# Optimization experiments

Hardware: AMD Instinct MI355X
Metric: run time of the kernel (lower is better)

The kernel has to match this reference:

```python
import jax, jax.numpy as jnp
import numpy as np

B, T, D, H, O = 16, 1024, 128, 1024, 64
ALPHA = 0.1  # leak rate of the leaky firing-rate cell


def setup_inputs() -> dict:
    key = jax.random.key(0)
    ks = jax.random.split(key, 9)
    s_in, s_rec = 1.0 / np.sqrt(D), 1.0 / np.sqrt(H)
    return {
        "x": jax.random.normal(ks[0], (B, T, D), dtype=jnp.float32),
        "W_in0": jax.random.normal(ks[1], (H, D), dtype=jnp.float32) * s_in,
        "W_rec0": jax.random.normal(ks[2], (H, H), dtype=jnp.float32) * s_rec,
        "b0": jnp.zeros((H,), dtype=jnp.float32),
        "W_in1": jax.random.normal(ks[3], (H, H), dtype=jnp.float32) * s_rec,
        "W_rec1": jax.random.normal(ks[4], (H, H), dtype=jnp.float32) * s_rec,
        "b1": jnp.zeros((H,), dtype=jnp.float32),
        "W_out": jax.random.normal(ks[5], (O, H), dtype=jnp.float32) * s_rec,
        "b_out": jnp.zeros((O,), dtype=jnp.float32),
    }


def reference(x, W_in0, W_rec0, b0, W_in1, W_rec1, b1, W_out, b_out):
    bs = x.shape[0]
    h = W_rec0.shape[0]
    fr0 = jnp.zeros((bs, h), x.dtype)  # init states (torch.zeros layer_states[:,0])
    v0 = jnp.zeros((bs, h), x.dtype)
    fr1 = jnp.zeros((bs, h), x.dtype)
    v1 = jnp.zeros((bs, h), x.dtype)

    def cell(fr, v, u, W_in, W_rec, b):
        # leaky integration: v <- (1-a)v + a(W_in u + W_rec fr + b); fr = tanh(v)
        v_new = (1.0 - ALPHA) * v + ALPHA * (u @ W_in.T + fr @ W_rec.T + b)
        return jnp.tanh(v_new), v_new

    def step(carry, x_t):
        fr0, v0, fr1, v1 = carry
        fr0, v0 = cell(fr0, v0, x_t, W_in0, W_rec0, b0)
        fr1, v1 = cell(fr1, v1, fr0, W_in1, W_rec1, b1)
        return (fr0, v0, fr1, v1), (fr0, fr1)

    xs = jnp.swapaxes(x, 0, 1)  # [T, B, D] for scan over time
    _, (s0, s1) = jax.lax.scan(step, (fr0, v0, fr1, v1), xs)
    states0 = jnp.swapaxes(s0, 0, 1)  # [B, T, H]
    states1 = jnp.swapaxes(s1, 0, 1)  # [B, T, H]
    output = states1 @ W_out.T + b_out  # readout on last layer's state sequence
    return (output, states0, states1)
```

## Files before the change

### kernel.cpp

```cpp
#include <hip/hip_runtime.h>

#define B_ 16
#define T_ 1024
#define D_ 128
#define H_ 1024
#define O_ 64
#define ALPHA_ 0.1f
#define LEAK_ 0.9f
#define GRID_SCAN 256

typedef float f32x4 __attribute__((ext_vector_type(4)));

__global__ __launch_bounds__(256)
void p0_kernel(const float* __restrict__ X, const float* __restrict__ Win0,
               const float* __restrict__ b0, float* __restrict__ P)
{
    __shared__ float Xs[64][68];
    __shared__ float Ws[64][68];
    const int r0 = blockIdx.x * 64;
    const int j0 = blockIdx.y * 64;
    const int tid = threadIdx.x;
    const int ty = tid >> 4, tx = tid & 15;
    float acc[4][4] = {};

    for (int kc = 0; kc < D_; kc += 64) {
        for (int i = tid; i < 64 * 16; i += 256) {
            int row = i >> 4, c = i & 15;
            *(float4*)&Xs[row][c * 4] =
                *(const float4*)&X[(size_t)(r0 + row) * D_ + kc + c * 4];
            *(float4*)&Ws[row][c * 4] =
                *(const float4*)&Win0[(size_t)(j0 + row) * D_ + kc + c * 4];
        }
        __syncthreads();
        #pragma unroll 4
        for (int k = 0; k < 64; k += 4) {
            float4 xr[4], wv[4];
            #pragma unroll
            for (int i = 0; i < 4; ++i) {
                xr[i] = *(const float4*)&Xs[ty * 4 + i][k];
                wv[i] = *(const float4*)&Ws[tx * 4 + i][k];
            }
            #pragma unroll
            for (int i = 0; i < 4; ++i)
                #pragma unroll
                for (int j = 0; j < 4; ++j) {
                    acc[i][j] = fmaf(xr[i].x, wv[j].x, acc[i][j]);
                    acc[i][j] = fmaf(xr[i].y, wv[j].y, acc[i][j]);
                    acc[i][j] = fmaf(xr[i].z, wv[j].z, acc[i][j]);
                    acc[i][j] = fmaf(xr[i].w, wv[j].w, acc[i][j]);
                }
        }
        __syncthreads();
    }
    #pragma unroll
    for (int i = 0; i < 4; ++i) {
        size_t r = (size_t)(r0 + ty * 4 + i);
        #pragma unroll
        for (int j = 0; j < 4; ++j) {
            int jj = j0 + tx * 4 + j;
            P[r * H_ + jj] = ALPHA_ * (acc[i][j] + b0[jj]);
        }
    }
}

#define LDX4(dst, p) \
    asm volatile("global_load_dwordx4 %0, %1, off" : "=v"(dst) : "v"(p))
#define LDSC(dst, p) \
    asm volatile("global_load_dword %0, %1, off sc0 sc1" : "=v"(dst) : "v"(p))
#define VMWAIT(n) asm volatile("s_waitcnt vmcnt(" #n ")" ::: "memory")
#define SB0 __builtin_amdgcn_sched_barrier(0)

#define POLL(ptr, tgtv) do {                                               \
    for (;;) {                                                             \
        unsigned pv_;                                                      \
        LDSC(pv_, (ptr));                                                  \
        VMWAIT(0);                                                         \
        if (__all((int)(pv_ >= (tgtv)))) break;                            \
        __builtin_amdgcn_s_sleep(1);                                       \
    }                                                                      \
    SB0;                                                                   \
} while (0)

#define FMA_A(Ar, r) do {                                                  \
    _Pragma("unroll")                                                      \
    for (int m_ = 0; m_ < 4; ++m_)                                         \
        _Pragma("unroll")                                                  \
        for (int c_ = 0; c_ < 4; ++c_) {                                   \
            const int kk_ = m_ * 4 + c_;                                   \
            const float xa_ = Ar[m_][c_];                                  \
            _Pragma("unroll")                                              \
            for (int j_ = 0; j_ < 4; ++j_) {                               \
                acc0[(r)*4+j_] = fmaf(xa_, wr0[j_][kk_], acc0[(r)*4+j_]);  \
                acc1[(r)*4+j_] = fmaf(xa_, wi1[j_][kk_], acc1[(r)*4+j_]);  \
            }                                                              \
        }                                                                  \
} while (0)

#define FMA_B(Br, r) do {                                                  \
    _Pragma("unroll")                                                      \
    for (int m_ = 0; m_ < 4; ++m_)                                         \
        _Pragma("unroll")                                                  \
        for (int c_ = 0; c_ < 4; ++c_) {                                   \
            const int kk_ = m_ * 4 + c_;                                   \
            const float xb_ = Br[m_][c_];                                  \
            _Pragma("unroll")                                              \
            for (int j_ = 0; j_ < 4; ++j_)                                 \
                acc1[(r)*4+j_] = fmaf(xb_, wr1[j_][kk_], acc1[(r)*4+j_]);  \
        }                                                                  \
} while (0)

__global__ __launch_bounds__(256, 1)
void scan_kernel(const float* __restrict__ Wr0,
                 const float* __restrict__ Wi1,
                 const float* __restrict__ Wr1,
                 const float* __restrict__ b1,
                 float* __restrict__ states0,
                 float* __restrict__ states1,
                 unsigned int* __restrict__ flags)
{
    const int tid  = threadIdx.x;
    const int xcd  = blockIdx.x & 7;
    const int slot = blockIdx.x >> 3;
    const int bg   = xcd >> 1;
    const int jg   = slot * 2 + (xcd & 1);
    const int lane = tid & 63;
    const int w    = tid >> 6;
    const int jq   = lane & 3;
    const int kl   = lane >> 2;
    const int ks   = w * 16 + kl;
    const int k0   = ks << 4;
    const int jbase = jg * 16 + jq * 4;
    const size_t BT = (size_t)T_ * H_;

    float wr0[4][16], wi1[4][16], wr1[4][16];
    #pragma unroll
    for (int j = 0; j < 4; ++j) {
        const float* p0 = Wr0 + (size_t)(jbase + j) * H_ + k0;
        const float* p1 = Wi1 + (size_t)(jbase + j) * H_ + k0;
        const float* p2 = Wr1 + (size_t)(jbase + j) * H_ + k0;
        #pragma unroll
        for (int m = 0; m < 4; ++m) {
            *(float4*)&wr0[j][m * 4] = ((const float4*)p0)[m];
            *(float4*)&wi1[j][m * 4] = ((const float4*)p1)[m];
            *(float4*)&wr1[j][m * 4] = ((const float4*)p2)[m];
        }
    }

    const int o      = tid & 63;
    const int b_loc  = o >> 4, j_loc = o & 15;
    const int gb     = bg * 4 + b_loc;
    const int gj     = jg * 16 + j_loc;
    const int otile  = j_loc >> 2;
    const int oa     = b_loc * 4 + (j_loc & 3);
    float v0 = 0.f, v1 = 0.f;
    const float b1v = b1[gj];

    __shared__ float red[2][4][4][16];

    unsigned* flag0 = flags;
    unsigned* flag1 = flags + 256;
    unsigned* myf0  = flag0 + bg * 64 + jg;
    unsigned* myf1  = flag1 + bg * 64 + jg;
    const unsigned* pf0 = flag0 + bg * 64 + lane;
    const unsigned* pf1 = flag1 + bg * 64 + lane;

    if (tid < 64) {
        size_t oidx = (size_t)gb * BT + gj;
        float pv;
        LDSC(pv, states0 + oidx);
        VMWAIT(0); SB0;
        v0 = pv;
        float fr = tanhf(v0);
        __hip_atomic_store(&states0[oidx], fr, __ATOMIC_RELAXED,
                           __HIP_MEMORY_SCOPE_AGENT);
        VMWAIT(0); SB0;
        if (tid == 0)
            __hip_atomic_store(myf0, 1u, __ATOMIC_RELAXED,
                               __HIP_MEMORY_SCOPE_AGENT);
    }

    for (int it = 1; it <= T_; ++it) {
        const unsigned tgt = (unsigned)it;

        POLL(pf0, tgt);

        float acc0[16], acc1[16];
        #pragma unroll
        for (int a = 0; a < 16; ++a) { acc0[a] = 0.f; acc1[a] = 0.f; }

        const float* sa = states0 + (size_t)(bg * 4) * BT
                        + (size_t)(it - 1) * H_ + k0;
        f32x4 A0[4], A1[4], A2[4], A3[4];
        LDX4(A0[0], sa);          LDX4(A0[1], sa + 4);
        LDX4(A0[2], sa + 8);      LDX4(A0[3], sa + 12);
        LDX4(A1[0], sa + BT);     LDX4(A1[1], sa + BT + 4);
        LDX4(A1[2], sa + BT + 8); LDX4(A1[3], sa + BT + 12);
        LDX4(A2[0], sa + 2*BT);     LDX4(A2[1], sa + 2*BT + 4);
        LDX4(A2[2], sa + 2*BT + 8); LDX4(A2[3], sa + 2*BT + 12);
        LDX4(A3[0], sa + 3*BT);     LDX4(A3[1], sa + 3*BT + 4);
        LDX4(A3[2], sa + 3*BT + 8); LDX4(A3[3], sa + 3*BT + 12);
        float pval = 0.f;
        size_t oidx0 = 0;
        if (tid < 64) {
            const int tp = (it < T_) ? it : (T_ - 1);
            oidx0 = (size_t)gb * BT + (size_t)tp * H_ + gj;
            LDSC(pval, states0 + oidx0);
        }
        VMWAIT(12); SB0;  FMA_A(A0, 0);
        VMWAIT(8);  SB0;  FMA_A(A1, 1);
        VMWAIT(4);  SB0;  FMA_A(A2, 2);
        VMWAIT(0);  SB0;  FMA_A(A3, 3);

        #pragma unroll
        for (int mask = 4; mask < 64; mask <<= 1)
            #pragma unroll
            for (int a = 0; a < 16; ++a)
                acc0[a] += __shfl_xor(acc0[a], mask);
        if (lane < 4)
            #pragma unroll
            for (int a = 0; a < 16; ++a)
                red[0][w][lane][a] = acc0[a];
        __syncthreads();

        if (tid < 64 && it < T_) {
            float s = red[0][0][otile][oa] + red[0][1][otile][oa]
                    + red[0][2][otile][oa] + red[0][3][otile][oa];
            v0 = LEAK_ * v0 + pval + ALPHA_ * s;
            float fr = tanhf(v0);
            __hip_atomic_store(&states0[oidx0], fr, __ATOMIC_RELAXED,
                               __HIP_MEMORY_SCOPE_AGENT);
            VMWAIT(0); SB0;
            if (tid == 0)
                __hip_atomic_store(myf0, (unsigned)(it + 1), __ATOMIC_RELAXED,
                                   __HIP_MEMORY_SCOPE_AGENT);
        }

        if (it >= 2) {
            POLL(pf1, tgt);
            const float* sb = states1 + (size_t)(bg * 4) * BT
                            + (size_t)(it - 2) * H_ + k0;
            f32x4 B0[4], B1r[4], B2r[4], B3r[4];
            LDX4(B0[0], sb);          LDX4(B0[1], sb + 4);
            LDX4(B0[2], sb + 8);      LDX4(B0[3], sb + 12);
            LDX4(B1r[0], sb + BT);     LDX4(B1r[1], sb + BT + 4);
            LDX4(B1r[2], sb + BT + 8); LDX4(B1r[3], sb + BT + 12);
            LDX4(B2r[0], sb + 2*BT);     LDX4(B2r[1], sb + 2*BT + 4);
            LDX4(B2r[2], sb + 2*BT + 8); LDX4(B2r[3], sb + 2*BT + 12);
            LDX4(B3r[0], sb + 3*BT);     LDX4(B3r[1], sb + 3*BT + 4);
            LDX4(B3r[2], sb + 3*BT + 8); LDX4(B3r[3], sb + 3*BT + 12);
            VMWAIT(12); SB0;  FMA_B(B0, 0);
            VMWAIT(8);  SB0;  FMA_B(B1r, 1);
            VMWAIT(4);  SB0;  FMA_B(B2r, 2);
            VMWAIT(0);  SB0;  FMA_B(B3r, 3);
        }

        #pragma unroll
        for (int mask = 4; mask < 64; mask <<= 1)
            #pragma unroll
            for (int a = 0; a < 16; ++a)
                acc1[a] += __shfl_xor(acc1[a], mask);
        if (lane < 4)
            #pragma unroll
            for (int a = 0; a < 16; ++a)
                red[1][w][lane][a] = acc1[a];
        __syncthreads();

        if (tid >= 64 && tid < 128) {
            float s = red[1][0][otile][oa] + red[1][1][otile][oa]
                    + red[1][2][otile][oa] + red[1][3][otile][oa];
            v1 = LEAK_ * v1 + ALPHA_ * (s + b1v);
            float fr = tanhf(v1);
            __hip_atomic_store(&states1[(size_t)gb * BT + (size_t)(it - 1) * H_ + gj],
                               fr, __ATOMIC_RELAXED, __HIP_MEMORY_SCOPE_AGENT);
            VMWAIT(0); SB0;
            if (tid == 64)
                __hip_atomic_store(myf1, (unsigned)(it + 1), __ATOMIC_RELAXED,
                                   __HIP_MEMORY_SCOPE_AGENT);
        }
    }
}

__global__ __launch_bounds__(256)
void out_kernel(const float* __restrict__ S1, const float* __restrict__ Wout,
                const float* __restrict__ bout, float* __restrict__ Out)
{
    __shared__ float Ss[64][36];
    __shared__ float Ws[64][36];
    const int r0 = blockIdx.x * 64;
    const int tid = threadIdx.x;
    const int ty = tid >> 4, tx = tid & 15;
    float acc[4][4] = {};

    for (int kc = 0; kc < H_; kc += 32) {
        for (int i = tid; i < 64 * 8; i += 256) {
            int row = i >> 3, c = i & 7;
            *(float4*)&Ss[row][c * 4] =
                *(const float4*)&S1[(size_t)(r0 + row) * H_ + kc + c * 4];
            *(float4*)&Ws[row][c * 4] =
                *(const float4*)&Wout[(size_t)row * H_ + kc + c * 4];
        }
        __syncthreads();
        #pragma unroll 2
        for (int k = 0; k < 32; k += 4) {
            float4 xr[4], wv[4];
            #pragma unroll
            for (int i = 0; i < 4; ++i) {
                xr[i] = *(const float4*)&Ss[ty * 4 + i][k];
                wv[i] = *(const float4*)&Ws[tx * 4 + i][k];
            }
            #pragma unroll
            for (int i = 0; i < 4; ++i)
                #pragma unroll
                for (int j = 0; j < 4; ++j) {
                    acc[i][j] = fmaf(xr[i].x, wv[j].x, acc[i][j]);
                    acc[i][j] = fmaf(xr[i].y, wv[j].y, acc[i][j]);
                    acc[i][j] = fmaf(xr[i].z, wv[j].z, acc[i][j]);
                    acc[i][j] = fmaf(xr[i].w, wv[j].w, acc[i][j]);
                }
        }
        __syncthreads();
    }
    #pragma unroll
    for (int i = 0; i < 4; ++i) {
        size_t r = (size_t)(r0 + ty * 4 + i);
        #pragma unroll
        for (int j = 0; j < 4; ++j) {
            int oo = tx * 4 + j;
            Out[r * O_ + oo] = acc[i][j] + bout[oo];
        }
    }
}

extern "C" void kernel_launch(void* const* d_in, const int* in_sizes, int n_in,
                              void* d_out, int out_size, void* d_ws, size_t ws_size,
                              hipStream_t stream)
{
    (void)in_sizes; (void)n_in; (void)out_size; (void)ws_size;

    const float* x    = (const float*)d_in[0];
    const float* Win0 = (const float*)d_in[1];
    const float* Wr0  = (const float*)d_in[2];
    const float* b0   = (const float*)d_in[3];
    const float* Wi1  = (const float*)d_in[4];
    const float* Wr1  = (const float*)d_in[5];
    const float* b1   = (const float*)d_in[6];
    const float* Wout = (const float*)d_in[7];
    const float* bout = (const float*)d_in[8];

    float* out     = (float*)d_out;
    float* states0 = out + (size_t)B_ * T_ * O_;
    float* states1 = states0 + (size_t)B_ * T_ * H_;

    unsigned* flags = (unsigned*)d_ws;

    hipMemsetAsync(d_ws, 0, 512 * sizeof(unsigned), stream);

    p0_kernel<<<dim3(B_ * T_ / 64, H_ / 64), 256, 0, stream>>>(x, Win0, b0, states0);

    scan_kernel<<<dim3(GRID_SCAN), dim3(256), 0, stream>>>(
        Wr0, Wi1, Wr1, b1, states0, states1, flags);

    out_kernel<<<dim3(B_ * T_ / 64), 256, 0, stream>>>(states1, Wout, bout, out);
}
```

Baseline: 4.977 ms.

## Split recurrent scan into separate layer-0 and layer-1 block groups

Doubles the scan grid and gives each layer its own set of persistent blocks. Layer-0 blocks only do the W_rec0 matvec and publish states0. Layer-1 blocks poll both flag sets and then do the W_in1 and W_rec1 products, so layer 1 trails layer 0 in a pipeline instead of sitting on its serial path. The costs are twice as many co-resident blocks (launch bounds raised to 2 per CU) and extra cross-block flag polling; if all blocks cannot be resident at once, the spin-waits could deadlock.

```diff
diff --git a/kernel.cpp b/kernel.cpp
--- a/kernel.cpp
+++ b/kernel.cpp
@@ -7,7 +7,7 @@
 #define O_ 64
 #define ALPHA_ 0.1f
 #define LEAK_ 0.9f
-#define GRID_SCAN 256
+#define GRID_SCAN 512
 
 typedef float f32x4 __attribute__((ext_vector_type(4)));
 
@@ -70,46 +70,54 @@
 #define VMWAIT(n) asm volatile("s_waitcnt vmcnt(" #n ")" ::: "memory")
 #define SB0 __builtin_amdgcn_sched_barrier(0)
 
-#define POLL(ptr, tgtv) do {                                               \
+#define POLL1F(pa_, tgtv) do {                                             \
     for (;;) {                                                             \
-        unsigned pv_;                                                      \
-        LDSC(pv_, (ptr));                                                  \
+        unsigned va_;                                                      \
+        LDSC(va_, (pa_));                                                  \
         VMWAIT(0);                                                         \
-        if (__all((int)(pv_ >= (tgtv)))) break;                            \
+        if (__all((int)(va_ >= (tgtv)))) break;                            \
         __builtin_amdgcn_s_sleep(1);                                       \
     }                                                                      \
     SB0;                                                                   \
 } while (0)
 
-#define FMA_A(Ar, r) do {                                                  \
+#define POLL2F(pa_, pb_, tgtv) do {                                        \
+    for (;;) {                                                             \
+        unsigned va_, vb_;                                                 \
+        LDSC(va_, (pa_));                                                  \
+        LDSC(vb_, (pb_));                                                  \
+        VMWAIT(0);                                                         \
+        if (__all((int)((va_ >= (tgtv)) & (vb_ >= (tgtv))))) break;        \
+        __builtin_amdgcn_s_sleep(1);                                       \
+    }                                                                      \
+    SB0;                                                                   \
+} while (0)
+
+#define FMA_G(Ar, r, W) do {                                               \
     _Pragma("unroll")                                                      \
     for (int m_ = 0; m_ < 4; ++m_)                                         \
         _Pragma("unroll")                                                  \
         for (int c_ = 0; c_ < 4; ++c_) {                                   \
             const int kk_ = m_ * 4 + c_;                                   \
-            const float xa_ = Ar[m_][c_];                                  \
+            const float x_ = Ar[m_][c_];                                   \
             _Pragma("unroll")                                              \
-            for (int j_ = 0; j_ < 4; ++j_) {                               \
-                acc0[(r)*4+j_] = fmaf(xa_, wr0[j_][kk_], acc0[(r)*4+j_]);  \
-                acc1[(r)*4+j_] = fmaf(xa_, wi1[j_][kk_], acc1[(r)*4+j_]);  \
-            }                                                              \
+            for (int j_ = 0; j_ < 4; ++j_)                                 \
+                acc[(r)*4+j_] = fmaf(x_, W[j_][kk_], acc[(r)*4+j_]);       \
         }                                                                  \
 } while (0)
 
-#define FMA_B(Br, r) do {                                                  \
-    _Pragma("unroll")                                                      \
-    for (int m_ = 0; m_ < 4; ++m_)                                         \
-        _Pragma("unroll")                                                  \
-        for (int c_ = 0; c_ < 4; ++c_) {                                   \
-            const int kk_ = m_ * 4 + c_;                                   \
-            const float xb_ = Br[m_][c_];                                  \
-            _Pragma("unroll")                                              \
-            for (int j_ = 0; j_ < 4; ++j_)                                 \
-                acc1[(r)*4+j_] = fmaf(xb_, wr1[j_][kk_], acc1[(r)*4+j_]);  \
-        }                                                                  \
+#define LOAD_ROWS(Rv, base) do {                                           \
+    LDX4(Rv##0[0], (base));              LDX4(Rv##0[1], (base) + 4);       \
+    LDX4(Rv##0[2], (base) + 8);          LDX4(Rv##0[3], (base) + 12);      \
+    LDX4(Rv##1[0], (base) + BT);         LDX4(Rv##1[1], (base) + BT + 4);  \
+    LDX4(Rv##1[2], (base) + BT + 8);     LDX4(Rv##1[3], (base) + BT + 12); \
+    LDX4(Rv##2[0], (base) + 2*BT);       LDX4(Rv##2[1], (base) + 2*BT + 4);\
+    LDX4(Rv##2[2], (base) + 2*BT + 8);   LDX4(Rv##2[3], (base) + 2*BT + 12);\
+    LDX4(Rv##3[0], (base) + 3*BT);       LDX4(Rv##3[1], (base) + 3*BT + 4);\
+    LDX4(Rv##3[2], (base) + 3*BT + 8);   LDX4(Rv##3[3], (base) + 3*BT + 12);\
 } while (0)
 
-__global__ __launch_bounds__(256, 1)
+__global__ __launch_bounds__(256, 2)
 void scan_kernel(const float* __restrict__ Wr0,
                  const float* __restrict__ Wi1,
                  const float* __restrict__ Wr1,
@@ -118,9 +126,12 @@
                  float* __restrict__ states1,
                  unsigned int* __restrict__ flags)
 {
-    const int tid  = threadIdx.x;
-    const int xcd  = blockIdx.x & 7;
-    const int slot = blockIdx.x >> 3;
+    const int tid   = threadIdx.x;
+    const int blk   = blockIdx.x;
+    const int eng   = blk >> 8;
+    const int inner = blk & 255;
+    const int xcd  = inner & 7;
+    const int slot = inner >> 3;
     const int bg   = xcd >> 1;
     const int jg   = slot * 2 + (xcd & 1);
     const int lane = tid & 63;
@@ -132,150 +143,166 @@
     const int jbase = jg * 16 + jq * 4;
     const size_t BT = (size_t)T_ * H_;
 
-    float wr0[4][16], wi1[4][16], wr1[4][16];
-    #pragma unroll
-    for (int j = 0; j < 4; ++j) {
-        const float* p0 = Wr0 + (size_t)(jbase + j) * H_ + k0;
-        const float* p1 = Wi1 + (size_t)(jbase + j) * H_ + k0;
-        const float* p2 = Wr1 + (size_t)(jbase + j) * H_ + k0;
-        #pragma unroll
-        for (int m = 0; m < 4; ++m) {
-            *(float4*)&wr0[j][m * 4] = ((const float4*)p0)[m];
-            *(float4*)&wi1[j][m * 4] = ((const float4*)p1)[m];
-            *(float4*)&wr1[j][m * 4] = ((const float4*)p2)[m];
-        }
-    }
-
     const int o      = tid & 63;
     const int b_loc  = o >> 4, j_loc = o & 15;
     const int gb     = bg * 4 + b_loc;
     const int gj     = jg * 16 + j_loc;
     const int otile  = j_loc >> 2;
     const int oa     = b_loc * 4 + (j_loc & 3);
-    float v0 = 0.f, v1 = 0.f;
-    const float b1v = b1[gj];
-
-    __shared__ float red[2][4][4][16];
+
+    __shared__ float red[4][4][16];
 
     unsigned* flag0 = flags;
     unsigned* flag1 = flags + 256;
-    unsigned* myf0  = flag0 + bg * 64 + jg;
-    unsigned* myf1  = flag1 + bg * 64 + jg;
     const unsigned* pf0 = flag0 + bg * 64 + lane;
     const unsigned* pf1 = flag1 + bg * 64 + lane;
 
-    if (tid < 64) {
-        size_t oidx = (size_t)gb * BT + gj;
-        float pv;
-        LDSC(pv, states0 + oidx);
-        VMWAIT(0); SB0;
-        v0 = pv;
-        float fr = tanhf(v0);
-        __hip_atomic_store(&states0[oidx], fr, __ATOMIC_RELAXED,
-                           __HIP_MEMORY_SCOPE_AGENT);
-        VMWAIT(0); SB0;
-        if (tid == 0)
-            __hip_atomic_store(myf0, 1u, __ATOMIC_RELAXED,
-                               __HIP_MEMORY_SCOPE_AGENT);
-    }
-
-    for (int it = 1; it <= T_; ++it) {
-        const unsigned tgt = (unsigned)it;
-
-        POLL(pf0, tgt);
-
-        float acc0[16], acc1[16];
+    if (eng == 0) {
+        float wr0[4][16];
         #pragma unroll
-        for (int a = 0; a < 16; ++a) { acc0[a] = 0.f; acc1[a] = 0.f; }
-
-        const float* sa = states0 + (size_t)(bg * 4) * BT
-                        + (size_t)(it - 1) * H_ + k0;
-        f32x4 A0[4], A1[4], A2[4], A3[4];
-        LDX4(A0[0], sa);          LDX4(A0[1], sa + 4);
-        LDX4(A0[2], sa + 8);      LDX4(A0[3], sa + 12);
-        LDX4(A1[0], sa + BT);     LDX4(A1[1], sa + BT + 4);
-        LDX4(A1[2], sa + BT + 8); LDX4(A1[3], sa + BT + 12);
-        LDX4(A2[0], sa + 2*BT);     LDX4(A2[1], sa + 2*BT + 4);
-        LDX4(A2[2], sa + 2*BT + 8); LDX4(A2[3], sa + 2*BT + 12);
-        LDX4(A3[0], sa + 3*BT);     LDX4(A3[1], sa + 3*BT + 4);
-        LDX4(A3[2], sa + 3*BT + 8); LDX4(A3[3], sa + 3*BT + 12);
-        float pval = 0.f;
-        size_t oidx0 = 0;
+        for (int j = 0; j < 4; ++j) {
+            const float* p0 = Wr0 + (size_t)(jbase + j) * H_ + k0;
+            #pragma unroll
+            for (int m = 0; m < 4; ++m)
+                *(float4*)&wr0[j][m * 4] = ((const float4*)p0)[m];
+        }
+        unsigned* myf0 = flag0 + bg * 64 + jg;
+        float v0 = 0.f;
+
         if (tid < 64) {
-            const int tp = (it < T_) ? it : (T_ - 1);
-            oidx0 = (size_t)gb * BT + (size_t)tp * H_ + gj;
-            LDSC(pval, states0 + oidx0);
-        }
-        VMWAIT(12); SB0;  FMA_A(A0, 0);
-        VMWAIT(8);  SB0;  FMA_A(A1, 1);
-        VMWAIT(4);  SB0;  FMA_A(A2, 2);
-        VMWAIT(0);  SB0;  FMA_A(A3, 3);
-
-        #pragma unroll
-        for (int mask = 4; mask < 64; mask <<= 1)
-            #pragma unroll
-            for (int a = 0; a < 16; ++a)
-                acc0[a] += __shfl_xor(acc0[a], mask);
-        if (lane < 4)
-            #pragma unroll
-            for (int a = 0; a < 16; ++a)
-                red[0][w][lane][a] = acc0[a];
-        __syncthreads();
-
-        if (tid < 64 && it < T_) {
-            float s = red[0][0][otile][oa] + red[0][1][otile][oa]
-                    + red[0][2][otile][oa] + red[0][3][otile][oa];
-            v0 = LEAK_ * v0 + pval + ALPHA_ * s;
+            size_t oidx = (size_t)gb * BT + gj;
+            float pv;
+            LDSC(pv, states0 + oidx);
+            VMWAIT(0); SB0;
+            v0 = pv;
             float fr = tanhf(v0);
-            __hip_atomic_store(&states0[oidx0], fr, __ATOMIC_RELAXED,
+            __hip_atomic_store(&states0[oidx], fr, __ATOMIC_RELAXED,
                                __HIP_MEMORY_SCOPE_AGENT);
             VMWAIT(0); SB0;
             if (tid == 0)
-                __hip_atomic_store(myf0, (unsigned)(it + 1), __ATOMIC_RELAXED,
+                __hip_atomic_store(myf0, 1u, __ATOMIC_RELAXED,
                                    __HIP_MEMORY_SCOPE_AGENT);
         }
 
-        if (it >= 2) {
-            POLL(pf1, tgt);
-            const float* sb = states1 + (size_t)(bg * 4) * BT
-                            + (size_t)(it - 2) * H_ + k0;
-            f32x4 B0[4], B1r[4], B2r[4], B3r[4];
-            LDX4(B0[0], sb);          LDX4(B0[1], sb + 4);
-            LDX4(B0[2], sb + 8);      LDX4(B0[3], sb + 12);
-            LDX4(B1r[0], sb + BT);     LDX4(B1r[1], sb + BT + 4);
-            LDX4(B1r[2], sb + BT + 8); LDX4(B1r[3], sb + BT + 12);
-            LDX4(B2r[0], sb + 2*BT);     LDX4(B2r[1], sb + 2*BT + 4);
-            LDX4(B2r[2], sb + 2*BT + 8); LDX4(B2r[3], sb + 2*BT + 12);
-            LDX4(B3r[0], sb + 3*BT);     LDX4(B3r[1], sb + 3*BT + 4);
-            LDX4(B3r[2], sb + 3*BT + 8); LDX4(B3r[3], sb + 3*BT + 12);
-            VMWAIT(12); SB0;  FMA_B(B0, 0);
-            VMWAIT(8);  SB0;  FMA_B(B1r, 1);
-            VMWAIT(4);  SB0;  FMA_B(B2r, 2);
-            VMWAIT(0);  SB0;  FMA_B(B3r, 3);
-        }
-
+        for (int it = 1; it < T_; ++it) {
+            POLL1F(pf0, (unsigned)it);
+
+            float acc[16];
+            #pragma unroll
+            for (int a = 0; a < 16; ++a) acc[a] = 0.f;
+
+            const float* sa = states0 + (size_t)(bg * 4) * BT
+                            + (size_t)(it - 1) * H_ + k0;
+            f32x4 A0[4], A1[4], A2[4], A3[4];
+            LOAD_ROWS(A, sa);
+            float pval = 0.f;
+            size_t oidx0 = 0;
+            if (tid < 64) {
+                oidx0 = (size_t)gb * BT + (size_t)it * H_ + gj;
+                LDSC(pval, states0 + oidx0);
+            }
+            VMWAIT(12); SB0;  FMA_G(A0, 0, wr0);
+            VMWAIT(8);  SB0;  FMA_G(A1, 1, wr0);
+            VMWAIT(4);  SB0;  FMA_G(A2, 2, wr0);
+            VMWAIT(0);  SB0;  FMA_G(A3, 3, wr0);
+
+            #pragma unroll
+            for (int mask = 4; mask < 64; mask <<= 1)
+                #pragma unroll
+                for (int a = 0; a < 16; ++a)
+                    acc[a] += __shfl_xor(acc[a], mask);
+            if (lane < 4)
+                #pragma unroll
+                for (int a = 0; a < 16; ++a)
+                    red[w][lane][a] = acc[a];
+            __syncthreads();
+
+            if (tid < 64) {
+                float s = red[0][otile][oa] + red[1][otile][oa]
+                        + red[2][otile][oa] + red[3][otile][oa];
+                v0 = LEAK_ * v0 + pval + ALPHA_ * s;
+                float fr = tanhf(v0);
+                __hip_atomic_store(&states0[oidx0], fr, __ATOMIC_RELAXED,
+                                   __HIP_MEMORY_SCOPE_AGENT);
+                VMWAIT(0); SB0;
+                if (tid == 0)
+                    __hip_atomic_store(myf0, (unsigned)(it + 1),
+                                       __ATOMIC_RELAXED,
+                                       __HIP_MEMORY_SCOPE_AGENT);
+            }
+        }
+    } else {
+        float wi1[4][16], wr1[4][16];
         #pragma unroll
-        for (int mask = 4; mask < 64; mask <<= 1)
-            #pragma unroll
-            for (int a = 0; a < 16; ++a)
-                acc1[a] += __shfl_xor(acc1[a], mask);
-        if (lane < 4)
-            #pragma unroll
-            for (int a = 0; a < 16; ++a)
-                red[1][w][lane][a] = acc1[a];
-        __syncthreads();
-
-        if (tid >= 64 && tid < 128) {
-            float s = red[1][0][otile][oa] + red[1][1][otile][oa]
-                    + red[1][2][otile][oa] + red[1][3][otile][oa];
-            v1 = LEAK_ * v1 + ALPHA_ * (s + b1v);
-            float fr = tanhf(v1);
-            __hip_atomic_store(&states1[(size_t)gb * BT + (size_t)(it - 1) * H_ + gj],
-                               fr, __ATOMIC_RELAXED, __HIP_MEMORY_SCOPE_AGENT);
-            VMWAIT(0); SB0;
-            if (tid == 64)
-                __hip_atomic_store(myf1, (unsigned)(it + 1), __ATOMIC_RELAXED,
+        for (int j = 0; j < 4; ++j) {
+            const float* p1 = Wi1 + (size_t)(jbase + j) * H_ + k0;
+            const float* p2 = Wr1 + (size_t)(jbase + j) * H_ + k0;
+            #pragma unroll
+            for (int m = 0; m < 4; ++m) {
+                *(float4*)&wi1[j][m * 4] = ((const float4*)p1)[m];
+                *(float4*)&wr1[j][m * 4] = ((const float4*)p2)[m];
+            }
+        }
+        unsigned* myf1 = flag1 + bg * 64 + jg;
+        float v1 = 0.f;
+        const float b1v = (tid < 64) ? b1[gj] : 0.f;
+
+        for (int it = 1; it <= T_; ++it) {
+            const unsigned tgt = (unsigned)it;
+            if (it >= 2) POLL2F(pf0, pf1, tgt);
+            else         POLL1F(pf0, tgt);
+
+            float acc[16];
+            #pragma unroll
+            for (int a = 0; a < 16; ++a) acc[a] = 0.f;
+
+            {
+                const float* sa = states0 + (size_t)(bg * 4) * BT
+                                + (size_t)(it - 1) * H_ + k0;
+                f32x4 A0[4], A1[4], A2[4], A3[4];
+                LOAD_ROWS(A, sa);
+                VMWAIT(12); SB0;  FMA_G(A0, 0, wi1);
+                VMWAIT(8);  SB0;  FMA_G(A1, 1, wi1);
+                VMWAIT(4);  SB0;  FMA_G(A2, 2, wi1);
+                VMWAIT(0);  SB0;  FMA_G(A3, 3, wi1);
+            }
+            if (it >= 2) {
+                const float* sb = states1 + (size_t)(bg * 4) * BT
+                                + (size_t)(it - 2) * H_ + k0;
+                f32x4 C0[4], C1[4], C2[4], C3[4];
+                LOAD_ROWS(C, sb);
+                VMWAIT(12); SB0;  FMA_G(C0, 0, wr1);
+                VMWAIT(8);  SB0;  FMA_G(C1, 1, wr1);
+                VMWAIT(4);  SB0;  FMA_G(C2, 2, wr1);
+                VMWAIT(0);  SB0;  FMA_G(C3, 3, wr1);
+            }
+
+            #pragma unroll
+            for (int mask = 4; mask < 64; mask <<= 1)
+                #pragma unroll
+                for (int a = 0; a < 16; ++a)
+                    acc[a] += __shfl_xor(acc[a], mask);
+            if (lane < 4)
+                #pragma unroll
+                for (int a = 0; a < 16; ++a)
+                    red[w][lane][a] = acc[a];
+            __syncthreads();
+
+            if (tid < 64) {
+                float s = red[0][otile][oa] + red[1][otile][oa]
+                        + red[2][otile][oa] + red[3][otile][oa];
+                v1 = LEAK_ * v1 + ALPHA_ * (s + b1v);
+                float fr = tanhf(v1);
+                __hip_atomic_store(&states1[(size_t)gb * BT
+                                            + (size_t)(it - 1) * H_ + gj],
+                                   fr, __ATOMIC_RELAXED,
                                    __HIP_MEMORY_SCOPE_AGENT);
+                VMWAIT(0); SB0;
+                if (tid == 0)
+                    __hip_atomic_store(myf1, (unsigned)(it + 1),
+                                       __ATOMIC_RELAXED,
+                                       __HIP_MEMORY_SCOPE_AGENT);
+            }
         }
     }
 }
```

After: 14.42 ms. +189.8%, slower.
